# Kernel tuning notes

Measured on AMD Instinct MI355X. Metric: run time of the kernel, lower is better.

## Reference

```python
import jax, jax.numpy as jnp
import numpy as np

E = 19   # electrodes
H = 32   # lstm hidden dim per direction


def setup_inputs() -> dict:
    key = jax.random.key(0)
    ks = jax.random.split(key, 8)
    B, T = 64, 2048
    s = 1.0 / np.sqrt(H)  # PyTorch LSTM/Linear init scale
    u = lambda k, shp: jax.random.uniform(k, shp, jnp.float32, -s, s)
    return {
        "x": jax.random.normal(ks[0], (B, T, E), jnp.float32),
        # per-electrode, per-direction LSTM params (input_dim=1 so w_ih is a vector per gate block)
        "w_ih": u(ks[1], (E, 2, 4 * H)),          # [E, dir, 4H]
        "w_hh": u(ks[2], (E, 2, 4 * H, H)),       # [E, dir, 4H, H]
        "b_ih": u(ks[3], (E, 2, 4 * H)),
        "b_hh": u(ks[4], (E, 2, 4 * H)),
        "ln_gamma": jnp.ones((E, 2 * H), jnp.float32),
        "ln_beta": jnp.zeros((E, 2 * H), jnp.float32),
        "fc_w": u(ks[5], (1, 2 * H)),
        "fc_b": u(ks[6], (1,)),
    }


def reference(x, w_ih, w_hh, b_ih, b_hh, ln_gamma, ln_beta, fc_w, fc_b):
    B, T, E_ = x.shape
    # dir 0 = forward time, dir 1 = reversed time (bidirectional)
    xs = jnp.stack([x, x[:, ::-1, :]], axis=-1)      # [B, T, E, 2]
    xs = jnp.moveaxis(xs, 1, 0)                      # [T, B, E, 2]
    b = b_ih + b_hh                                  # [E, 2, 4H]

    h0 = jnp.zeros((B, E_, 2, H), x.dtype)
    c0 = jnp.zeros_like(h0)

    def step(carry, xt):
        h, c = carry
        # xt: [B, E, 2] scalar input per electrode/direction (input_dim == 1)
        gates = xt[..., None] * w_ih + jnp.einsum('bedh,edgh->bedg', h, w_hh) + b
        i, f, g, o = jnp.split(gates, 4, axis=-1)    # PyTorch gate order i,f,g,o
        c = jax.nn.sigmoid(f) * c + jax.nn.sigmoid(i) * jnp.tanh(g)
        h = jax.nn.sigmoid(o) * jnp.tanh(c)
        return (h, c), None

    (hT, _), _ = jax.lax.scan(step, (h0, c0), xs)
    # final hidden: dir0 = fwd at t=T-1 (hn[-2]), dir1 = bwd at t=0 (hn[-1]); concat features
    out = hT.reshape(B, E_, 2 * H)                   # [B, E, 64]

    # per-electrode LayerNorm over the 64-dim feature
    mu = out.mean(-1, keepdims=True)
    var = out.var(-1, keepdims=True)
    out = (out - mu) / jnp.sqrt(var + 1e-5) * ln_gamma + ln_beta

    pooled = out.mean(axis=1)                        # mean over electrodes -> [B, 64]
    logits = pooled @ fc_w.T + fc_b                  # [B, 1]
    return logits[:, 0]
```

## Files before the change

kernel.cpp:

```cpp
#include <hip/hip_runtime.h>
#include <math.h>
#include <stdint.h>

#define E_N 19
#define H_N 32
#define T_N 2048
#define B_N 64
#define G_N 128
#define XCHUNK 64
#define LOG2E 1.4426950408889634f

typedef _Float16 half2_t __attribute__((ext_vector_type(2)));

__device__ __forceinline__ float lanef(float v, int l) {
    return __int_as_float(__builtin_amdgcn_readlane(__float_as_int(v), l));
}
__device__ __forceinline__ uint32_t laneu(uint32_t v, int l) {
    return (uint32_t)__builtin_amdgcn_readlane((int)v, l);
}
__device__ __forceinline__ float sigm_rcp(float e) {
    return __builtin_amdgcn_rcpf(1.0f + e);
}

__global__ __launch_bounds__(64)
__attribute__((amdgpu_waves_per_eu(3, 3)))
void lstm_chain_kernel(
    const float* __restrict__ x,
    const float* __restrict__ w_ih,
    const float* __restrict__ w_hh,
    const float* __restrict__ b_ih,
    const float* __restrict__ b_hh,
    float* __restrict__ hT)
{
    const int lane  = threadIdx.x;
    const int chain = blockIdx.x;
    const int b  = chain / (E_N * 2);
    const int ed = chain - b * (E_N * 2);
    const int e  = ed >> 1;
    const int d  = ed & 1;
    const int j    = lane & 31;
    const int half = lane >> 5;

    const int r1 = j + 64 * half;
    const int r2 = j + 32 + 64 * half;

    const float* wr1 = w_hh + ((size_t)ed * G_N + r1) * H_N;
    const float* wr2 = w_hh + ((size_t)ed * G_N + r2) * H_N;
    uint32_t w1p[16], w2p[16];
    #pragma unroll
    for (int m = 0; m < 16; ++m) {
        float2 v1 = ((const float2*)wr1)[m];
        float2 v2 = ((const float2*)wr2)[m];
        half2_t p1 = { (_Float16)v1.x, (_Float16)v1.y };
        half2_t p2 = { (_Float16)v2.x, (_Float16)v2.y };
        w1p[m] = __builtin_bit_cast(uint32_t, p1);
        w2p[m] = __builtin_bit_cast(uint32_t, p2);
    }

    const float wih1  = w_ih[(size_t)ed * G_N + r1];
    const float wih2  = w_ih[(size_t)ed * G_N + r2];
    const float bias1 = b_ih[(size_t)ed * G_N + r1] + b_hh[(size_t)ed * G_N + r1];
    const float bias2 = b_ih[(size_t)ed * G_N + r2] + b_hh[(size_t)ed * G_N + r2];

    const float K1 = half ? (-2.0f * LOG2E) : (-LOG2E);
    const float A1 = half ?  2.0f :  1.0f;
    const float B1 = half ? -1.0f :  0.0f;

    uint32_t sh[16];
    #pragma unroll
    for (int m = 0; m < 16; ++m) sh[m] = 0u;

    float c = 0.0f;
    float h = 0.0f;

    const float* xbase = x + (size_t)b * T_N * E_N + e;

    for (int t0 = 0; t0 < T_N; t0 += XCHUNK) {
        #pragma unroll
        for (int m = 0; m < 16; ++m) {
            asm volatile("" : "+v"(w1p[m]), "+v"(w2p[m]));
        }

        const int tt    = t0 + lane;
        const int tphys = d ? (T_N - 1 - tt) : tt;
        const float xr  = xbase[(size_t)tphys * E_N];

        #pragma unroll 1
        for (int tl = 0; tl < XCHUNK; ++tl) {
            const float sx = lanef(xr, tl);

            float a1 = fmaf(sx, wih1, bias1), a1b = 0.0f;
            float a2 = fmaf(sx, wih2, bias2), a2b = 0.0f;
            #pragma unroll
            for (int m = 0; m < 8; ++m) {
                a1  = __builtin_amdgcn_fdot2(__builtin_bit_cast(half2_t, sh[m]),
                                             __builtin_bit_cast(half2_t, w1p[m]),   a1,  false);
                a1b = __builtin_amdgcn_fdot2(__builtin_bit_cast(half2_t, sh[m+8]),
                                             __builtin_bit_cast(half2_t, w1p[m+8]), a1b, false);
                a2  = __builtin_amdgcn_fdot2(__builtin_bit_cast(half2_t, sh[m]),
                                             __builtin_bit_cast(half2_t, w2p[m]),   a2,  false);
                a2b = __builtin_amdgcn_fdot2(__builtin_bit_cast(half2_t, sh[m+8]),
                                             __builtin_bit_cast(half2_t, w2p[m+8]), a2b, false);
            }
            const float g1 = a1 + a1b;
            const float g2 = a2 + a2b;

            const float e1   = __builtin_amdgcn_exp2f(g1 * K1);
            const float act1 = fmaf(A1, sigm_rcp(e1), B1);
            const float e2   = __builtin_amdgcn_exp2f(g2 * (-LOG2E));
            const float act2 = sigm_rcp(e2);

            const float oth1 = __shfl_xor(act1, 32);
            const float oth2 = __shfl_xor(act2, 32);

            const float ig = act1 * oth1;
            const float fv = half ? oth2 : act2;
            const float ov = half ? act2 : oth2;

            c = fmaf(fv, c, ig);
            const float ec = __builtin_amdgcn_exp2f(c * (-2.0f * LOG2E));
            const float tc = fmaf(2.0f, sigm_rcp(ec), -1.0f);
            h = ov * tc;

            const _Float16 hh = (_Float16)h;
            const uint32_t hlo = (uint32_t)__builtin_bit_cast(uint16_t, hh);
            const uint32_t nb  = (uint32_t)__shfl_down((int)hlo, 1);
            const uint32_t pk  = hlo | (nb << 16);
            #pragma unroll
            for (int m = 0; m < 16; ++m) sh[m] = laneu(pk, 2 * m);
        }
    }

    if (!half) {
        hT[((size_t)(b * E_N + e) * 2 + d) * H_N + j] = h;
    }
}

__global__ __launch_bounds__(64) void head_kernel(
    const float* __restrict__ hT,
    const float* __restrict__ ln_gamma,
    const float* __restrict__ ln_beta,
    const float* __restrict__ fc_w,
    const float* __restrict__ fc_b,
    float* __restrict__ out)
{
    const int b = blockIdx.x;
    const int f = threadIdx.x;

    float acc = 0.0f;
    for (int e = 0; e < E_N; ++e) {
        const float v = hT[(size_t)(b * E_N + e) * 64 + f];
        float s = v, s2 = v * v;
        #pragma unroll
        for (int off = 32; off > 0; off >>= 1) {
            s  += __shfl_xor(s,  off);
            s2 += __shfl_xor(s2, off);
        }
        const float mean = s * (1.0f / 64.0f);
        const float var  = s2 * (1.0f / 64.0f) - mean * mean;
        const float inv  = rsqrtf(var + 1e-5f);
        acc += (v - mean) * inv * ln_gamma[e * 64 + f] + ln_beta[e * 64 + f];
    }
    float contrib = (acc * (1.0f / (float)E_N)) * fc_w[f];
    #pragma unroll
    for (int off = 32; off > 0; off >>= 1) contrib += __shfl_xor(contrib, off);
    if (f == 0) out[b] = contrib + fc_b[0];
}

extern "C" void kernel_launch(void* const* d_in, const int* in_sizes, int n_in,
                              void* d_out, int out_size, void* d_ws, size_t ws_size,
                              hipStream_t stream) {
    const float* x        = (const float*)d_in[0];
    const float* w_ih     = (const float*)d_in[1];
    const float* w_hh     = (const float*)d_in[2];
    const float* b_ih     = (const float*)d_in[3];
    const float* b_hh     = (const float*)d_in[4];
    const float* ln_gamma = (const float*)d_in[5];
    const float* ln_beta  = (const float*)d_in[6];
    const float* fc_w     = (const float*)d_in[7];
    const float* fc_b     = (const float*)d_in[8];
    float* out = (float*)d_out;
    float* hT  = (float*)d_ws;

    lstm_chain_kernel<<<B_N * E_N * 2, 64, 0, stream>>>(x, w_ih, w_hh, b_ih, b_hh, hT);
    head_kernel<<<B_N, 64, 0, stream>>>(hT, ln_gamma, ln_beta, fc_w, fc_b, out);
}
```

Baseline: 1.104 ms.

## Remap LSTM gate rows across half-waves to cut cross-lane shuffles per step

Result: slower. 1.287 ms (+16.6%).

```diff
diff --git a/kernel.cpp b/kernel.cpp
--- a/kernel.cpp
+++ b/kernel.cpp
@@ -41,8 +41,8 @@
     const int j    = lane & 31;
     const int half = lane >> 5;
 
-    const int r1 = j + 64 * half;
-    const int r2 = j + 32 + 64 * half;
+    const int r1 = j + 32 * half;
+    const int r2 = j + 64 + 32 * half;
 
     const float* wr1 = w_hh + ((size_t)ed * G_N + r1) * H_N;
     const float* wr2 = w_hh + ((size_t)ed * G_N + r2) * H_N;
@@ -62,9 +62,9 @@
     const float bias1 = b_ih[(size_t)ed * G_N + r1] + b_hh[(size_t)ed * G_N + r1];
     const float bias2 = b_ih[(size_t)ed * G_N + r2] + b_hh[(size_t)ed * G_N + r2];
 
-    const float K1 = half ? (-2.0f * LOG2E) : (-LOG2E);
-    const float A1 = half ?  2.0f :  1.0f;
-    const float B1 = half ? -1.0f :  0.0f;
+    const float K2 = half ? (-LOG2E) : (-2.0f * LOG2E);
+    const float A2 = half ?  1.0f :  2.0f;
+    const float B2 = half ?  0.0f : -1.0f;
 
     uint32_t sh[16];
     #pragma unroll
@@ -105,33 +105,28 @@
             const float g1 = a1 + a1b;
             const float g2 = a2 + a2b;
 
-            const float e1   = __builtin_amdgcn_exp2f(g1 * K1);
-            const float act1 = fmaf(A1, sigm_rcp(e1), B1);
-            const float e2   = __builtin_amdgcn_exp2f(g2 * (-LOG2E));
-            const float act2 = sigm_rcp(e2);
+            const float act1 = sigm_rcp(__builtin_amdgcn_exp2f(g1 * (-LOG2E)));
+            const float act2 = fmaf(A2, sigm_rcp(__builtin_amdgcn_exp2f(g2 * K2)), B2);
 
-            const float oth1 = __shfl_xor(act1, 32);
-            const float oth2 = __shfl_xor(act2, 32);
+            const float ig  = act1 * act2;
+            const float igx = __shfl_xor(ig, 32);
 
-            const float ig = act1 * oth1;
-            const float fv = half ? oth2 : act2;
-            const float ov = half ? act2 : oth2;
+            c = fmaf(act1, c, igx);
+            const float tc = fmaf(2.0f, sigm_rcp(
+                __builtin_amdgcn_exp2f(c * (-2.0f * LOG2E))), -1.0f);
+            h = act2 * tc;
 
-            c = fmaf(fv, c, ig);
-            const float ec = __builtin_amdgcn_exp2f(c * (-2.0f * LOG2E));
-            const float tc = fmaf(2.0f, sigm_rcp(ec), -1.0f);
-            h = ov * tc;
-
-            const _Float16 hh = (_Float16)h;
-            const uint32_t hlo = (uint32_t)__builtin_bit_cast(uint16_t, hh);
-            const uint32_t nb  = (uint32_t)__shfl_down((int)hlo, 1);
-            const uint32_t pk  = hlo | (nb << 16);
+            const uint32_t hu = (uint32_t)__builtin_bit_cast(uint16_t, (_Float16)h);
             #pragma unroll
-            for (int m = 0; m < 16; ++m) sh[m] = laneu(pk, 2 * m);
+            for (int m = 0; m < 16; ++m) {
+                const uint32_t lo = laneu(hu, 32 + 2 * m);
+                const uint32_t hi = laneu(hu, 33 + 2 * m);
+                sh[m] = lo | (hi << 16);
+            }
         }
     }
 
-    if (!half) {
+    if (half) {
         hT[((size_t)(b * E_N + e) * 2 + d) * H_N + j] = h;
     }
 }
```
